# Performance work log

Measured on AMD Instinct MI355X. Metric: run time of the kernel, lower is better.

Reference implementation:

```python
import jax, jax.numpy as jnp
import numpy as np

EPS = 1e-8


def _conv3x3(x, w, b):
    # x: [B,Ci,H,W], w: [Co,Ci,3,3], 'SAME' padding (stride 1)
    y = jax.lax.conv_general_dilated(x, w, (1, 1), 'SAME',
        dimension_numbers=('NCHW', 'OIHW', 'NCHW'))
    return y + b[None, :, None, None]


def _box3(x):
    # depthwise 3x3 box-sum with zero padding (uniform-kernel masked conv)
    C = x.shape[1]
    k = jnp.ones((C, 1, 3, 3), x.dtype)
    return jax.lax.conv_general_dilated(x, k, (1, 1), 'SAME',
        dimension_numbers=('NCHW', 'OIHW', 'NCHW'), feature_group_count=C)


def _unfold3(x):
    # stack_channel(1,9,k=3,p=1): x [B,1,H,W] -> 9 shifted copies [B,9,H,W]
    H, W = x.shape[-2:]
    xp = jnp.pad(x, ((0, 0), (0, 0), (1, 1), (1, 1)))
    return jnp.concatenate([xp[:, :, i:i + H, j:j + W]
                            for i in range(3) for j in range(3)], axis=1)


def _entropy(x):
    # generate_entropy: sigmoid(neighbor - center) averaged over the 3x3 patch
    # x: [B,1,H,W] -> [B,H,W]
    return jax.nn.sigmoid(_unfold3(x) - x).mean(axis=1)


def _pwf(x, params):
    # PixelWeightedFusionSoftmax: 1x1-conv + ReLU chain 2C->128->32->8->1
    for w, b in params:
        x = jax.nn.relu(jnp.einsum('oc,bchw->bohw', w, x) + b[None, :, None, None])
    return x


def _forward(bevs, compress_w, compress_b, pwf_params):
    BT, N, C, H, W = bevs.shape
    tg = bevs[:, 0]                                    # ego agent  [BT,C,H,W]
    nb = bevs[:, 1:].reshape(BT * (N - 1), C, H, W)    # neighbors

    # myCompressNet: 64 -> 1 channel
    tg_com = jax.nn.relu(_conv3x3(tg, compress_w, compress_b))   # [BT,1,H,W]
    nb_com = jax.nn.relu(_conv3x3(nb, compress_w, compress_b))   # [BT*(N-1),1,H,W]

    tg_ent = _entropy(tg_com)                                    # [BT,H,W]
    nb_ent = _entropy(nb_com).reshape(BT, N - 1, H, W)

    # attention_collaboration: select pixels where neighbor entropy exceeds ego's
    mask = (nb_ent > tg_ent[:, None]).astype(bevs.dtype)         # [BT,N-1,H,W]
    bandwidth = mask.mean()                                      # count / (H*W), averaged

    # conv_mask_uniform / interplot_f: partial conv w/ uniform 3x3 kernel
    m = mask.reshape(BT * (N - 1), 1, H, W)
    num = _box3(nb * m)                                          # [BT*(N-1),C,H,W]
    den = _box3(m)
    inter = num / (den + EPS)
    warp = m * nb + (1.0 - m) * inter

    # all-zero neighbors (min+max==0) are passed through untouched
    is_zero = (nb.min(axis=(1, 2, 3)) + nb.max(axis=(1, 2, 3))) == 0
    warp = jnp.where(is_zero[:, None, None, None], nb, warp)

    feats = jnp.concatenate([tg[:, None], warp.reshape(BT, N - 1, C, H, W)],
                            axis=1)                              # [BT,N,C,H,W]

    # per-agent pixel weights: exp / sum-exp normalize, then weighted fusion
    cat = jnp.concatenate([jnp.broadcast_to(tg[:, None], feats.shape), feats],
                          axis=2)                                # [BT,N,2C,H,W]
    logits = _pwf(cat.reshape(BT * N, 2 * C, H, W), pwf_params)
    logits = logits.reshape(BT, N, 1, H, W)
    wts = jnp.exp(logits)
    wts = wts / wts.sum(axis=1, keepdims=True)
    fused = (wts * feats).sum(axis=1)                            # [BT,C,H,W]
    return fused, bandwidth


def setup_inputs() -> dict:
    key = jax.random.key(0)
    ks = jax.random.split(key, 6)
    BT, N, C, H, W = 3, 5, 64, 200, 200
    s = 0.05
    return {
        'bevs': jax.random.normal(ks[0], (BT, N, C, H, W), jnp.float32),
        'compress_w': jax.random.normal(ks[1], (1, C, 3, 3), jnp.float32) * s,
        'compress_b': jnp.zeros((1,), jnp.float32),
        'pwf_w1': jax.random.normal(ks[2], (128, 2 * C), jnp.float32) * s,
        'pwf_b1': jnp.zeros((128,), jnp.float32),
        'pwf_w2': jax.random.normal(ks[3], (32, 128), jnp.float32) * s,
        'pwf_b2': jnp.zeros((32,), jnp.float32),
        'pwf_w3': jax.random.normal(ks[4], (8, 32), jnp.float32) * s,
        'pwf_b3': jnp.zeros((8,), jnp.float32),
        'pwf_w4': jax.random.normal(ks[5], (1, 8), jnp.float32) * s,
        'pwf_b4': jnp.zeros((1,), jnp.float32),
    }


def reference(bevs, compress_w, compress_b, pwf_w1, pwf_b1, pwf_w2, pwf_b2,
              pwf_w3, pwf_b3, pwf_w4, pwf_b4):
    pwf = [(pwf_w1, pwf_b1), (pwf_w2, pwf_b2), (pwf_w3, pwf_b3), (pwf_w4, pwf_b4)]
    return _forward(bevs, compress_w, compress_b, pwf)
```

## Files before the change

kernel.cpp:

```cpp
#include <hip/hip_runtime.h>
#include <hip/hip_bf16.h>
#include <math.h>

#define PP 40000
#define HDIM 200
#define WDIM 200
#define NEPS 1e-8f
#define GX 157
#define NPART (GX*12)

#define OFF_COM    0
#define OFF_ENT    (15*PP)
#define OFF_MASK   (30*PP)
#define OFF_DEN    (42*PP)
#define OFF_LOGITS (54*PP)
#define OFF_MISC   (69*PP)
#define OFF_XTG_F  (69*PP + 64)
#define OFF_XFT_F  (OFF_XTG_F + 3*PP*32)
#define OFF_WBF_F  (OFF_XFT_F + 12*PP*32)
#define OFF_CNT_F  (OFF_WBF_F + 10240)
#define WS_NEED ((size_t)(OFF_CNT_F + NPART + 64)*4)

typedef __attribute__((ext_vector_type(8))) short bf16x8;
typedef __attribute__((ext_vector_type(4))) float f32x4;

__device__ __forceinline__ short f2bf(float f){
    __hip_bfloat16 h = __float2bfloat16(f);
    return *reinterpret_cast<short*>(&h);
}
__device__ __forceinline__ float bf2f(short s){
    return __uint_as_float(((unsigned)(unsigned short)s) << 16);
}

__device__ __forceinline__ unsigned f2ord(float f){
    unsigned u = __float_as_uint(f);
    return (u & 0x80000000u) ? ~u : (u | 0x80000000u);
}
__device__ __forceinline__ float ord2f(unsigned u){
    unsigned v = (u & 0x80000000u) ? (u & 0x7fffffffu) : ~u;
    return __uint_as_float(v);
}

__device__ __forceinline__ void tap_setup(int p, int* off, bool* val){
    int h = p / WDIM, w = p - h*WDIM;
#pragma unroll
    for (int ky=0;ky<3;ky++)
#pragma unroll
        for (int kx=0;kx<3;kx++){
            int t = ky*3+kx;
            int hh = h+ky-1, ww = w+kx-1;
            val[t] = (hh>=0)&&(hh<HDIM)&&(ww>=0)&&(ww<WDIM);
            int hc = min(max(hh,0),HDIM-1);
            int wc = min(max(ww,0),WDIM-1);
            off[t] = hc*WDIM+wc;
        }
}

__global__ void k_init(unsigned* misc){
    int t = threadIdx.x;
    if (t < 12) misc[t] = 0xFFFFFFFFu;
    else if (t < 25) misc[t] = 0u;
}

__global__ __launch_bounds__(256) void k_wcvt(const float* __restrict__ w1,
        const float* __restrict__ w2, short* __restrict__ wbf)
{
    int i = blockIdx.x*256 + threadIdx.x;
    if (i < 16384){
        int e = i&7, l = (i>>3)&63, ks = (i>>9)&3, nt = i>>11;
        int ln = l&15, kg = l>>4;
        wbf[i] = f2bf(w1[(nt*16+ln)*128 + ks*32 + kg*8 + e]);
    } else if (i < 20480){
        int j = i - 16384;
        int e = j&7, l = (j>>3)&63, ks = (j>>9)&3, nt2 = j>>11;
        int ln = l&15, kg = l>>4;
        wbf[i] = f2bf(w2[(nt2*16+ln)*128 + ks*32 + kg*8 + e]);
    }
}

__global__ __launch_bounds__(256) void k_csum(const float* __restrict__ bevs,
        const float* __restrict__ cw, unsigned* __restrict__ misc,
        float* __restrict__ z)
{
    int img = blockIdx.y;
    int n = img % 5;
    int idx = blockIdx.x*256 + threadIdx.x;
    bool act = idx < PP/4;
    int p = idx*4;
    float vmin = INFINITY, vmax = -INFINITY;
    f32x4 acc[9];
#pragma unroll
    for (int t=0;t<9;t++) acc[t] = (f32x4){0.f,0.f,0.f,0.f};
    if (act){
        const float* src = bevs + (size_t)img*64*PP;
#pragma unroll 2
        for (int c=0;c<64;c++){
            f32x4 v = *(const f32x4*)&src[(size_t)c*PP + p];
            vmin = fminf(fminf(fminf(vmin, v[0]), fminf(v[1], v[2])), v[3]);
            vmax = fmaxf(fmaxf(fmaxf(vmax, v[0]), fmaxf(v[1], v[2])), v[3]);
#pragma unroll
            for (int t=0;t<9;t++){
                float w = cw[c*9+t];
#pragma unroll
                for (int j=0;j<4;j++) acc[t][j] = fmaf(w, v[j], acc[t][j]);
            }
        }
        float* zimg = z + (size_t)img*9*PP;
#pragma unroll
        for (int t=0;t<9;t++)
            *(f32x4*)&zimg[(size_t)t*PP + p] = acc[t];
    }
    if (n > 0){
#pragma unroll
        for (int s=32;s>0;s>>=1){
            vmin = fminf(vmin, __shfl_xor(vmin, s, 64));
            vmax = fmaxf(vmax, __shfl_xor(vmax, s, 64));
        }
        if ((threadIdx.x & 63) == 0){
            int im12 = (img/5)*4 + (n-1);
            atomicMin(&misc[im12], f2ord(vmin));
            atomicMax(&misc[12+im12], f2ord(vmax));
        }
    }
}

__global__ __launch_bounds__(256) void k_cfin(const float* __restrict__ z,
        const float* __restrict__ cb, float* __restrict__ com)
{
    int img = blockIdx.y;
    int p = blockIdx.x*256 + threadIdx.x;
    if (p >= PP) return;
    int off[9]; bool val[9];
    tap_setup(p, off, val);
    const float* zimg = z + (size_t)img*9*PP;
    float v[9];
#pragma unroll
    for (int t=0;t<9;t++) v[t] = zimg[(size_t)t*PP + off[t]];
    float acc = cb[0];
#pragma unroll
    for (int t=0;t<9;t++) acc += val[t] ? v[t] : 0.0f;
    com[(size_t)img*PP + p] = fmaxf(acc, 0.0f);
}

__global__ __launch_bounds__(256) void k_conv(const float* __restrict__ bevs,
        const float* __restrict__ cw, const float* __restrict__ cb,
        float* __restrict__ com, unsigned* __restrict__ misc)
{
    int img = blockIdx.y;
    int n = img % 5;
    int p = blockIdx.x*256 + threadIdx.x;
    float vmin = INFINITY, vmax = -INFINITY;
    if (p < PP){
        int off[9]; bool val[9];
        tap_setup(p, off, val);
        const float* src = bevs + (size_t)img*64*PP;
        float acc = cb[0];
#pragma unroll 2
        for (int c=0;c<64;c++){
            const float* sc = src + (size_t)c*PP;
            float v[9];
#pragma unroll
            for (int t=0;t<9;t++) v[t] = sc[off[t]];
            vmin = fminf(vmin, v[4]); vmax = fmaxf(vmax, v[4]);
#pragma unroll
            for (int t=0;t<9;t++)
                acc = fmaf(cw[c*9+t], val[t] ? v[t] : 0.0f, acc);
        }
        com[(size_t)img*PP + p] = fmaxf(acc, 0.0f);
    }
    if (n > 0){
#pragma unroll
        for (int s=32;s>0;s>>=1){
            vmin = fminf(vmin, __shfl_xor(vmin, s, 64));
            vmax = fmaxf(vmax, __shfl_xor(vmax, s, 64));
        }
        if ((threadIdx.x & 63) == 0){
            int im12 = (img/5)*4 + (n-1);
            atomicMin(&misc[im12], f2ord(vmin));
            atomicMax(&misc[12+im12], f2ord(vmax));
        }
    }
}

__global__ __launch_bounds__(256) void k_ent(const float* __restrict__ com,
        float* __restrict__ ent)
{
    int img = blockIdx.y;
    int p = blockIdx.x*256 + threadIdx.x;
    if (p >= PP) return;
    int off[9]; bool val[9];
    tap_setup(p, off, val);
    const float* s = com + (size_t)img*PP;
    float x = s[p];
    float v[9];
#pragma unroll
    for (int t=0;t<9;t++) v[t] = s[off[t]];
    float acc = 0.0f;
#pragma unroll
    for (int t=0;t<9;t++){
        float xv = val[t] ? v[t] : 0.0f;
        acc += 1.0f/(1.0f + expf(x - xv));
    }
    ent[(size_t)img*PP + p] = acc / 9.0f;
}

__global__ __launch_bounds__(256) void k_maskp(const float* __restrict__ ent,
        float* __restrict__ maskb, unsigned* __restrict__ partial)
{
    __shared__ unsigned cnt[4];
    int im12 = blockIdx.y; int bt = im12 >> 2; int n = (im12 & 3) + 1;
    int p = blockIdx.x*256 + threadIdx.x;
    int v = 0;
    if (p < PP){
        float en = ent[(size_t)(bt*5+n)*PP + p];
        float et = ent[(size_t)(bt*5)*PP + p];
        v = en > et;
        maskb[(size_t)im12*PP + p] = (float)v;
    }
    unsigned long long bal = __ballot(v);
    if ((threadIdx.x & 63) == 0) cnt[threadIdx.x>>6] = (unsigned)__popcll(bal);
    __syncthreads();
    if (threadIdx.x == 0)
        partial[blockIdx.y*GX + blockIdx.x] = cnt[0]+cnt[1]+cnt[2]+cnt[3];
}

__global__ __launch_bounds__(256) void k_mask(const float* __restrict__ ent,
        float* __restrict__ maskb, unsigned* __restrict__ misc)
{
    int im12 = blockIdx.y; int bt = im12 >> 2; int n = (im12 & 3) + 1;
    int p = blockIdx.x*256 + threadIdx.x;
    int v = 0;
    if (p < PP){
        float en = ent[(size_t)(bt*5+n)*PP + p];
        float et = ent[(size_t)(bt*5)*PP + p];
        v = en > et;
        maskb[(size_t)im12*PP + p] = (float)v;
    }
    unsigned long long bal = __ballot(v);
    if ((threadIdx.x & 63) == 0) atomicAdd(&misc[24], (unsigned)__popcll(bal));
}

__global__ __launch_bounds__(256) void k_den(const float* __restrict__ maskb,
        float* __restrict__ denb)
{
    int im12 = blockIdx.y;
    int p = blockIdx.x*256 + threadIdx.x;
    if (p >= PP) return;
    int off[9]; bool val[9];
    tap_setup(p, off, val);
    const float* mrow = maskb + (size_t)im12*PP;
    float v[9];
#pragma unroll
    for (int t=0;t<9;t++) v[t] = mrow[off[t]];
    float s = 0.0f;
#pragma unroll
    for (int t=0;t<9;t++) s += val[t] ? v[t] : 0.0f;
    denb[(size_t)im12*PP + p] = s;
}

__global__ __launch_bounds__(256) void k_finp(const unsigned* __restrict__ partial,
        unsigned* misc, float* bwout)
{
    __shared__ unsigned sh[4];
    unsigned s = 0;
    for (int i = threadIdx.x; i < NPART; i += 256) s += partial[i];
#pragma unroll
    for (int sft=32;sft>0;sft>>=1) s += (unsigned)__shfl_xor((int)s, sft, 64);
    if ((threadIdx.x & 63) == 0) sh[threadIdx.x>>6] = s;
    __syncthreads();
    int t = threadIdx.x;
    if (t < 12){
        float mn = ord2f(misc[t]);
        float mx = ord2f(misc[12+t]);
        ((int*)misc)[25+t] = (mn + mx == 0.0f) ? 1 : 0;
    }
    if (t == 12) bwout[0] = (float)(sh[0]+sh[1]+sh[2]+sh[3]) / 480000.0f;
}

__global__ void k_fin(unsigned* misc, float* bwout){
    int t = threadIdx.x;
    if (t < 12){
        float mn = ord2f(misc[t]);
        float mx = ord2f(misc[12+t]);
        ((int*)misc)[25+t] = (mn + mx == 0.0f) ? 1 : 0;
    }
    if (t == 12) bwout[0] = (float)misc[24] / 480000.0f;
}

__global__ __launch_bounds__(256) void k_xtg(const float* __restrict__ bevs,
        short* __restrict__ Xtg)
{
    __shared__ short tile[64][72];
    int tid = threadIdx.x;
    int bt = blockIdx.y;
    int px0 = blockIdx.x*64;
    const float* tg = bevs + (size_t)bt*5*64*PP;
    int c = tid>>2, q = tid&3;
#pragma unroll
    for (int j=0;j<4;j++){
        int pxl = q*16 + j*4;
        f32x4 v = *(const f32x4*)&tg[(size_t)c*PP + px0 + pxl];
#pragma unroll
        for (int e=0;e<4;e++) tile[pxl+e][c] = f2bf(v[e]);
    }
    __syncthreads();
    int pxl = tid&63, qq = tid>>6;
    short* base = Xtg + (size_t)bt*PP*64;
    *(bf16x8*)&base[((size_t)(2*qq  )*PP + px0 + pxl)*8] = *(bf16x8*)&tile[pxl][qq*16];
    *(bf16x8*)&base[((size_t)(2*qq+1)*PP + px0 + pxl)*8] = *(bf16x8*)&tile[pxl][qq*16+8];
}

__global__ __launch_bounds__(256) void k_xft(const float* __restrict__ bevs,
        const float* __restrict__ maskb,
        const unsigned* __restrict__ misc, short* __restrict__ Xft)
{
    int im12 = blockIdx.y; int bt = im12 >> 2; int n = (im12 & 3) + 1;
    int chunk = blockIdx.z;
    int chb = chunk*8;
    int idx = blockIdx.x*256 + threadIdx.x;
    if (idx >= PP/4) return;
    int p = idx*4;
    int row = p / WDIM, col0 = p - row*WDIM;
    int s0 = max(col0-4, 0), s2 = min(col0+4, WDIM-4);
    int rowc[3]; bool rowok[3];
#pragma unroll
    for (int r=0;r<3;r++){
        int rr = row + r - 1;
        rowok[r] = (rr>=0) && (rr<HDIM);
        rowc[r] = min(max(rr,0),HDIM-1) * WDIM;
    }
    bool colok[6];
#pragma unroll
    for (int k=0;k<6;k++){
        int cc = col0 + k - 1;
        colok[k] = (cc>=0) && (cc<WDIM);
    }
    const float* mrow = maskb + (size_t)im12*PP;
    float m6[3][6];
#pragma unroll
    for (int r=0;r<3;r++){
        f32x4 a0 = *(const f32x4*)&mrow[rowc[r] + s0];
        f32x4 a1 = *(const f32x4*)&mrow[rowc[r] + col0];
        f32x4 a2 = *(const f32x4*)&mrow[rowc[r] + s2];
        float mv[6] = {a0[3], a1[0], a1[1], a1[2], a1[3], a2[0]};
#pragma unroll
        for (int k=0;k<6;k++)
            m6[r][k] = (rowok[r] && colok[k]) ? mv[k] : 0.0f;
    }
    float rden[4];
#pragma unroll
    for (int j=0;j<4;j++){
        float d = 0.0f;
#pragma unroll
        for (int r=0;r<3;r++){
#pragma unroll
            for (int dk=0;dk<3;dk++) d += m6[r][j+dk];
        }
        rden[j] = 1.0f/(d + NEPS);
    }
    int iz = ((const int*)misc)[25+im12];
    const float* nbb = bevs + (size_t)(bt*5+n)*64*PP;

    short fv0[8], fv1[8], fv2[8], fv3[8];
#pragma unroll
    for (int ci=0;ci<8;ci++){
        int c = chb + ci;
        const float* sc = nbb + (size_t)c*PP;
        f32x4 v0[3], v1[3], v2[3];
#pragma unroll
        for (int r=0;r<3;r++){
            v0[r] = *(const f32x4*)&sc[rowc[r] + s0];
            v1[r] = *(const f32x4*)&sc[rowc[r] + col0];
            v2[r] = *(const f32x4*)&sc[rowc[r] + s2];
        }
        float num[4];
#pragma unroll
        for (int j=0;j<4;j++) num[j] = 0.0f;
#pragma unroll
        for (int r=0;r<3;r++){
            float vv[6] = {v0[r][3], v1[r][0], v1[r][1], v1[r][2], v1[r][3], v2[r][0]};
#pragma unroll
            for (int j=0;j<4;j++){
#pragma unroll
                for (int dk=0;dk<3;dk++)
                    num[j] = fmaf(m6[r][j+dk], vv[j+dk], num[j]);
            }
        }
        short out4[4];
#pragma unroll
        for (int j=0;j<4;j++){
            float center = v1[1][j];
            float mc = m6[1][j+1];
            float xc = iz ? center : fmaf(mc, center, (1.0f-mc)*(num[j]*rden[j]));
            out4[j] = f2bf(xc);
        }
        fv0[ci]=out4[0]; fv1[ci]=out4[1]; fv2[ci]=out4[2]; fv3[ci]=out4[3];
    }
    short* xc0 = Xft + (size_t)im12*PP*64 + ((size_t)chunk*PP + p)*8;
    *(bf16x8*)&xc0[0]  = *(bf16x8*)&fv0[0];
    *(bf16x8*)&xc0[8]  = *(bf16x8*)&fv1[0];
    *(bf16x8*)&xc0[16] = *(bf16x8*)&fv2[0];
    *(bf16x8*)&xc0[24] = *(bf16x8*)&fv3[0];
}

__global__ __launch_bounds__(256) void k_mlp(const short* __restrict__ Xtg,
        const short* __restrict__ Xft, const short* __restrict__ wbf,
        const float* __restrict__ b1, const float* __restrict__ b2,
        const float* __restrict__ w3, const float* __restrict__ b3,
        const float* __restrict__ w4, const float* __restrict__ b4,
        float* __restrict__ logits)
{
    __shared__ __align__(16) short w1t[16384];
    __shared__ __align__(16) short xt2[4*16*136];
    __shared__ __align__(16) float z2[4*16*33];
    __shared__ float b1l[128], b2l[32], b3l[8], w3l[8*33], w4l[8], b4l[1];

    int tid = threadIdx.x;
    int img = blockIdx.y, bt = img/5, n = img%5;

#pragma unroll
    for (int k=0;k<8;k++){
        int i = tid + k*256;
        *(bf16x8*)&w1t[i*8] = *(const bf16x8*)&wbf[i*8];
    }
    if (tid<256) w3l[(tid>>5)*33 + (tid&31)] = w3[tid];
    if (tid<128) b1l[tid]=b1[tid];
    if (tid<32)  b2l[tid]=b2[tid];
    if (tid<8)   b3l[tid]=b3[tid];
    if (tid<8)   w4l[tid]=w4[tid];
    if (tid==0)  b4l[0]=b4[0];

    int w = tid>>6, l = tid&63;
    int ln = l&15, kg = l>>4;

    bf16x8 w2f[2][4];
#pragma unroll
    for (int nt2=0;nt2<2;nt2++)
#pragma unroll
    for (int ks=0;ks<4;ks++)
        w2f[nt2][ks] = *(const bf16x8*)&wbf[16384 + ((nt2*4+ks)*64 + l)*8];

    __syncthreads();

    const short* xtgb = Xtg + (size_t)bt*PP*64;
    const short* xftb = (n>0) ? (Xft + (size_t)(bt*4+n-1)*PP*64) : xtgb;
    short* xt2w = &xt2[w*16*136];
    float* z2w  = &z2[w*16*33];
    int px_base = blockIdx.x*256 + w*64;

#pragma unroll 1
    for (int mt=0; mt<4; mt++){
        int prow = px_base + mt*16;
        int arow = prow + ln; if (arow > PP-1) arow = PP-1;
        bf16x8 af[4];
        af[0] = *(const bf16x8*)&xtgb[((size_t)kg*PP     + arow)*8];
        af[1] = *(const bf16x8*)&xtgb[((size_t)(kg+4)*PP + arow)*8];
        af[2] = *(const bf16x8*)&xftb[((size_t)kg*PP     + arow)*8];
        af[3] = *(const bf16x8*)&xftb[((size_t)(kg+4)*PP + arow)*8];

#pragma unroll
        for (int nt=0;nt<8;nt++){
            float bias = b1l[nt*16 + ln];
            f32x4 acc = {bias, bias, bias, bias};
#pragma unroll
            for (int ks=0;ks<4;ks++){
                bf16x8 bf = *(const bf16x8*)&w1t[((nt*4+ks)*64 + l)*8];
                acc = __builtin_amdgcn_mfma_f32_16x16x32_bf16(af[ks], bf, acc, 0, 0, 0);
            }
#pragma unroll
            for (int r=0;r<4;r++)
                xt2w[(kg*4+r)*136 + nt*16 + ln] = f2bf(fmaxf(acc[r], 0.0f));
        }

        bf16x8 a2[4];
#pragma unroll
        for (int ks=0;ks<4;ks++)
            a2[ks] = *(const bf16x8*)&xt2w[ln*136 + ks*32 + kg*8];
#pragma unroll
        for (int nt2=0;nt2<2;nt2++){
            float bias = b2l[nt2*16 + ln];
            f32x4 acc = {bias, bias, bias, bias};
#pragma unroll
            for (int ks=0;ks<4;ks++)
                acc = __builtin_amdgcn_mfma_f32_16x16x32_bf16(a2[ks], w2f[nt2][ks], acc, 0, 0, 0);
#pragma unroll
            for (int r=0;r<4;r++)
                z2w[(kg*4+r)*33 + nt2*16 + ln] = fmaxf(acc[r], 0.0f);
        }

        int k0 = kg*2, k1 = kg*2+1;
        float y0 = b3l[k0], y1 = b3l[k1];
#pragma unroll
        for (int j=0;j<32;j++){
            float v = z2w[ln*33 + j];
            y0 = fmaf(w3l[k0*33+j], v, y0);
            y1 = fmaf(w3l[k1*33+j], v, y1);
        }
        float part = w4l[k0]*fmaxf(y0,0.0f) + w4l[k1]*fmaxf(y1,0.0f);
        part += __shfl_xor(part, 16, 64);
        part += __shfl_xor(part, 32, 64);
        if (kg == 0 && prow + ln < PP)
            logits[(size_t)img*PP + prow + ln] = fmaxf(part + b4l[0], 0.0f);
    }
}

__global__ __launch_bounds__(256) void k_fuse2(const float* __restrict__ bevs,
        const float* __restrict__ logits, const short* __restrict__ Xft,
        float* __restrict__ out)
{
    int bt = blockIdx.y;
    int cb = blockIdx.z*32;
    int chunk0 = cb>>3;
    int p = blockIdx.x*256 + threadIdx.x;
    if (p >= PP) return;
    float e[5], ssum = 0.0f;
#pragma unroll
    for (int nn=0;nn<5;nn++){ e[nn] = expf(logits[(size_t)(bt*5+nn)*PP + p]); ssum += e[nn]; }
    float rs = 1.0f/ssum;
    const float* tgb = bevs + (size_t)bt*5*64*PP;
    float acc[32];
    float w0 = e[0]*rs;
#pragma unroll
    for (int ci=0;ci<32;ci++) acc[ci] = w0*tgb[(size_t)(cb+ci)*PP + p];
#pragma unroll
    for (int k=0;k<4;k++){
        float wk = e[k+1]*rs;
        const short* Xim = Xft + (size_t)(bt*4+k)*PP*64;
#pragma unroll
        for (int c8=0;c8<4;c8++){
            bf16x8 v = *(const bf16x8*)&Xim[((size_t)(chunk0+c8)*PP + p)*8];
#pragma unroll
            for (int j=0;j<8;j++)
                acc[c8*8+j] = fmaf(wk, bf2f(v[j]), acc[c8*8+j]);
        }
    }
#pragma unroll
    for (int ci=0;ci<32;ci++)
        out[((size_t)bt*64 + cb+ci)*PP + p] = acc[ci];
}

__global__ __launch_bounds__(256) void k_pwf(const float* __restrict__ bevs,
        const float* __restrict__ w1, const float* __restrict__ b1,
        const float* __restrict__ w2, const float* __restrict__ b2,
        const float* __restrict__ w3, const float* __restrict__ b3,
        const float* __restrict__ w4, const float* __restrict__ b4,
        const float* __restrict__ maskb, const float* __restrict__ denb,
        const unsigned* __restrict__ misc, float* __restrict__ logits)
{
    __shared__ __align__(16) short w1t[128*136];
    __shared__ __align__(16) short w2t[32*136];
    __shared__ __align__(16) short xt[64*136];
    __shared__ __align__(16) float z2[64*33];
    __shared__ float b1l[128], b2l[32], b3l[8], w3l[256], w4l[8], b4l[1];

    int tid = threadIdx.x;
    int img = blockIdx.y, bt = img/5, n = img%5;

    for (int i=tid;i<16384;i+=256) w1t[(i>>7)*136 + (i&127)] = f2bf(w1[i]);
    for (int i=tid;i<4096;i+=256)  w2t[(i>>7)*136 + (i&127)] = f2bf(w2[i]);
    if (tid<128) b1l[tid]=b1[tid];
    if (tid<32)  b2l[tid]=b2[tid];
    if (tid<8)   b3l[tid]=b3[tid];
    if (tid<256) w3l[tid]=w3[tid];
    if (tid<8)   w4l[tid]=w4[tid];
    if (tid==0)  b4l[0]=b4[0];

    int px = tid&63, q = tid>>6;
    int p = blockIdx.x*64 + px;
    const float* tg = bevs + (size_t)bt*5*64*PP;
    if (n == 0){
#pragma unroll
        for (int ci=0;ci<16;ci++){
            int c = q*16+ci;
            short v = f2bf(tg[(size_t)c*PP + p]);
            xt[px*136 + c] = v;
            xt[px*136 + 64 + c] = v;
        }
    } else {
        int im12 = bt*4 + (n-1);
        int off[9]; bool val[9];
        tap_setup(p, off, val);
        const float* mrow = maskb + (size_t)im12*PP;
        float m9[9];
#pragma unroll
        for (int t=0;t<9;t++) m9[t] = val[t] ? mrow[off[t]] : 0.0f;
        float rden = 1.0f/(denb[(size_t)im12*PP + p] + NEPS);
        int iz = ((const int*)misc)[25+im12];
        float mc = m9[4];
        const float* nbb = bevs + (size_t)(bt*5+n)*64*PP;
#pragma unroll
        for (int ci=0;ci<16;ci++){
            int c = q*16+ci;
            xt[px*136 + c] = f2bf(tg[(size_t)c*PP + p]);
            const float* sc = nbb + (size_t)c*PP;
            float num = 0.0f, center = 0.0f;
#pragma unroll
            for (int t=0;t<9;t++){
                if (val[t]){
                    float v = sc[off[t]];
                    num = fmaf(m9[t], v, num);
                    if (t==4) center = v;
                }
            }
            float xc = iz ? center : fmaf(mc, center, (1.0f-mc)*(num*rden));
            xt[px*136 + 64 + c] = f2bf(xc);
        }
    }
    __syncthreads();

    int w = tid>>6, l = tid&63;
    int ln = l&15, kg = l>>4;
    bf16x8 af[4];
#pragma unroll
    for (int ks=0;ks<4;ks++)
        af[ks] = *(const bf16x8*)&xt[(w*16+ln)*136 + ks*32 + kg*8];
#pragma unroll
    for (int nt=0;nt<8;nt++){
        float bias = b1l[nt*16 + ln];
        f32x4 acc = {bias, bias, bias, bias};
#pragma unroll
        for (int ks=0;ks<4;ks++){
            bf16x8 bf = *(const bf16x8*)&w1t[(nt*16+ln)*136 + ks*32 + kg*8];
            acc = __builtin_amdgcn_mfma_f32_16x16x32_bf16(af[ks], bf, acc, 0, 0, 0);
        }
#pragma unroll
        for (int r=0;r<4;r++){
            int pr = w*16 + kg*4 + r;
            xt[pr*136 + nt*16 + ln] = f2bf(fmaxf(acc[r], 0.0f));
        }
    }
    bf16x8 a2[4];
#pragma unroll
    for (int ks=0;ks<4;ks++)
        a2[ks] = *(const bf16x8*)&xt[(w*16+ln)*136 + ks*32 + kg*8];
#pragma unroll
    for (int nt2=0;nt2<2;nt2++){
        float bias = b2l[nt2*16 + ln];
        f32x4 acc = {bias, bias, bias, bias};
#pragma unroll
        for (int ks=0;ks<4;ks++){
            bf16x8 bf = *(const bf16x8*)&w2t[(nt2*16+ln)*136 + ks*32 + kg*8];
            acc = __builtin_amdgcn_mfma_f32_16x16x32_bf16(a2[ks], bf, acc, 0, 0, 0);
        }
#pragma unroll
        for (int r=0;r<4;r++){
            int pr = w*16 + kg*4 + r;
            z2[pr*33 + nt2*16 + ln] = fmaxf(acc[r], 0.0f);
        }
    }
    __syncthreads();
    if (tid < 64){
        float y3[8];
#pragma unroll
        for (int k=0;k<8;k++) y3[k] = b3l[k];
        for (int j=0;j<32;j++){
            float v = z2[tid*33 + j];
#pragma unroll
            for (int k=0;k<8;k++) y3[k] = fmaf(w3l[k*32+j], v, y3[k]);
        }
        float sres = b4l[0];
#pragma unroll
        for (int k=0;k<8;k++) sres = fmaf(w4l[k], fmaxf(y3[k], 0.0f), sres);
        logits[(size_t)img*PP + blockIdx.x*64 + tid] = fmaxf(sres, 0.0f);
    }
}

__global__ __launch_bounds__(256) void k_fuse_old(const float* __restrict__ bevs,
        const float* __restrict__ logits, const float* __restrict__ maskb,
        const float* __restrict__ denb, const unsigned* __restrict__ misc,
        float* __restrict__ out)
{
    int bt = blockIdx.y;
    int p = blockIdx.x*256 + threadIdx.x;
    if (p >= PP) return;
    int off[9]; bool val[9];
    tap_setup(p, off, val);
    float e[5], ssum = 0.0f;
#pragma unroll
    for (int nn=0;nn<5;nn++){ e[nn] = expf(logits[(size_t)(bt*5+nn)*PP + p]); ssum += e[nn]; }
    float wts[5];
#pragma unroll
    for (int nn=0;nn<5;nn++) wts[nn] = e[nn] / ssum;
    float m9[4][9]; float rden[4]; int iz[4];
#pragma unroll
    for (int k=0;k<4;k++){
        int im12 = bt*4 + k;
        const float* mrow = maskb + (size_t)im12*PP;
#pragma unroll
        for (int t=0;t<9;t++) m9[k][t] = val[t] ? mrow[off[t]] : 0.0f;
        rden[k] = 1.0f/(denb[(size_t)im12*PP + p] + NEPS);
        iz[k] = ((const int*)misc)[25+im12];
    }
    const float* base = bevs + (size_t)bt*5*64*PP;
    for (int c=0;c<64;c++){
        float tgc = base[(size_t)c*PP + p];
        float fused = wts[0]*tgc;
#pragma unroll
        for (int k=0;k<4;k++){
            const float* sc = base + (size_t)(k+1)*64*PP + (size_t)c*PP;
            float num = 0.0f, center = 0.0f;
#pragma unroll
            for (int t=0;t<9;t++){
                if (val[t]){
                    float v = sc[off[t]];
                    num = fmaf(m9[k][t], v, num);
                    if (t==4) center = v;
                }
            }
            float mc = m9[k][4];
            float xc = iz[k] ? center : fmaf(mc, center, (1.0f-mc)*(num*rden[k]));
            fused = fmaf(wts[k+1], xc, fused);
        }
        out[((size_t)bt*64 + c)*PP + p] = fused;
    }
}

extern "C" void kernel_launch(void* const* d_in, const int* in_sizes, int n_in,
                              void* d_out, int out_size, void* d_ws, size_t ws_size,
                              hipStream_t stream)
{
    const float* bevs = (const float*)d_in[0];
    const float* cw  = (const float*)d_in[1];
    const float* cb  = (const float*)d_in[2];
    const float* w1  = (const float*)d_in[3];
    const float* b1  = (const float*)d_in[4];
    const float* w2  = (const float*)d_in[5];
    const float* b2  = (const float*)d_in[6];
    const float* w3  = (const float*)d_in[7];
    const float* b3  = (const float*)d_in[8];
    const float* w4  = (const float*)d_in[9];
    const float* b4  = (const float*)d_in[10];
    float* out = (float*)d_out;
    float* ws = (float*)d_ws;

    float* com    = ws + OFF_COM;
    float* ent    = ws + OFF_ENT;
    float* maskb  = ws + OFF_MASK;
    float* denb   = ws + OFF_DEN;
    float* logits = ws + OFF_LOGITS;
    unsigned* misc = (unsigned*)(ws + OFF_MISC);
    short* Xtg    = (short*)(ws + OFF_XTG_F);
    short* Xft    = (short*)(ws + OFF_XFT_F);
    short* wbf    = (short*)(ws + OFF_WBF_F);
    unsigned* cntp = (unsigned*)(ws + OFF_CNT_F);
    float* z      = (float*)(ws + OFF_XFT_F);

    dim3 blk(256,1,1);
    int gx = GX;
    bool big = ws_size >= WS_NEED;

    k_init<<<dim3(1),dim3(64),0,stream>>>(misc);
    if (big){
        k_wcvt<<<dim3(80),blk,0,stream>>>(w1,w2,wbf);
        k_csum<<<dim3((PP/4+255)/256,15),blk,0,stream>>>(bevs,cw,misc,z);
        k_cfin<<<dim3(gx,15),blk,0,stream>>>(z,cb,com);
        k_xtg <<<dim3(PP/64,3),blk,0,stream>>>(bevs,Xtg);
    } else {
        k_conv<<<dim3(gx,15),blk,0,stream>>>(bevs,cw,cb,com,misc);
    }
    k_ent <<<dim3(gx,15),blk,0,stream>>>(com,ent);
    if (big){
        k_maskp<<<dim3(gx,12),blk,0,stream>>>(ent,maskb,cntp);
        k_finp<<<dim3(1),blk,0,stream>>>(cntp, misc, out + (size_t)3*64*PP);
        k_xft  <<<dim3((PP/4+255)/256,12,8),blk,0,stream>>>(bevs,maskb,misc,Xft);
        k_mlp  <<<dim3(gx,15),blk,0,stream>>>(Xtg,Xft,wbf,b1,b2,w3,b3,w4,b4,logits);
        k_fuse2<<<dim3(gx,3,2),blk,0,stream>>>(bevs,logits,Xft,out);
    } else {
        k_mask<<<dim3(gx,12),blk,0,stream>>>(ent,maskb,misc);
        k_den <<<dim3(gx,12),blk,0,stream>>>(maskb,denb);
        k_fin <<<dim3(1),dim3(64),0,stream>>>(misc, out + (size_t)3*64*PP);
        k_pwf  <<<dim3(PP/64,15),blk,0,stream>>>(bevs,w1,b1,w2,b2,w3,b3,w4,b4,maskb,denb,misc,logits);
        k_fuse_old<<<dim3(gx,3),blk,0,stream>>>(bevs,logits,maskb,denb,misc,out);
    }
}
```

Measured before the change: 245.3 us.

## Fuse ego bf16 transpose into compress-sum kernel and stage mask rows in LDS

The separate k_xtg kernel is removed. The ego-agent bf16 channel-packed tensor is now written from inside k_csum, which already streams every channel of the ego image. This avoids a second full read of the ego features and one kernel launch. k_xft also loads the needed mask rows into shared memory once per block instead of doing three overlapping global vector loads per row per thread, at the cost of extra LDS and a barrier.

```diff
diff --git a/kernel.cpp b/kernel.cpp
--- a/kernel.cpp
+++ b/kernel.cpp
@@ -80,10 +80,10 @@
 
 __global__ __launch_bounds__(256) void k_csum(const float* __restrict__ bevs,
         const float* __restrict__ cw, unsigned* __restrict__ misc,
-        float* __restrict__ z)
+        float* __restrict__ z, short* __restrict__ Xtg)
 {
     int img = blockIdx.y;
-    int n = img % 5;
+    int n = img % 5, bt = img / 5;
     int idx = blockIdx.x*256 + threadIdx.x;
     bool act = idx < PP/4;
     int p = idx*4;
@@ -93,16 +93,32 @@
     for (int t=0;t<9;t++) acc[t] = (f32x4){0.f,0.f,0.f,0.f};
     if (act){
         const float* src = bevs + (size_t)img*64*PP;
-#pragma unroll 2
-        for (int c=0;c<64;c++){
-            f32x4 v = *(const f32x4*)&src[(size_t)c*PP + p];
-            vmin = fminf(fminf(fminf(vmin, v[0]), fminf(v[1], v[2])), v[3]);
-            vmax = fmaxf(fmaxf(fmaxf(vmax, v[0]), fmaxf(v[1], v[2])), v[3]);
-#pragma unroll
-            for (int t=0;t<9;t++){
-                float w = cw[c*9+t];
-#pragma unroll
-                for (int j=0;j<4;j++) acc[t][j] = fmaf(w, v[j], acc[t][j]);
+        short* xb0 = Xtg + (size_t)bt*PP*64 + (size_t)p*8;
+#pragma unroll 1
+        for (int cg=0; cg<8; cg++){
+            short tgs[4][8];
+#pragma unroll
+            for (int ci=0; ci<8; ci++){
+                int c = cg*8 + ci;
+                f32x4 v = *(const f32x4*)&src[(size_t)c*PP + p];
+                vmin = fminf(fminf(fminf(vmin, v[0]), fminf(v[1], v[2])), v[3]);
+                vmax = fmaxf(fmaxf(fmaxf(vmax, v[0]), fmaxf(v[1], v[2])), v[3]);
+#pragma unroll
+                for (int t=0;t<9;t++){
+                    float w = cw[c*9+t];
+#pragma unroll
+                    for (int j=0;j<4;j++) acc[t][j] = fmaf(w, v[j], acc[t][j]);
+                }
+                if (n == 0){
+#pragma unroll
+                    for (int j=0;j<4;j++) tgs[j][ci] = f2bf(v[j]);
+                }
+            }
+            if (n == 0){
+                short* xb = xb0 + (size_t)cg*PP*8;
+#pragma unroll
+                for (int j=0;j<4;j++)
+                    *(bf16x8*)&xb[j*8] = *(bf16x8*)&tgs[j][0];
             }
         }
         float* zimg = z + (size_t)img*9*PP;
@@ -287,41 +303,33 @@
     if (t == 12) bwout[0] = (float)misc[24] / 480000.0f;
 }
 
-__global__ __launch_bounds__(256) void k_xtg(const float* __restrict__ bevs,
-        short* __restrict__ Xtg)
-{
-    __shared__ short tile[64][72];
-    int tid = threadIdx.x;
-    int bt = blockIdx.y;
-    int px0 = blockIdx.x*64;
-    const float* tg = bevs + (size_t)bt*5*64*PP;
-    int c = tid>>2, q = tid&3;
-#pragma unroll
-    for (int j=0;j<4;j++){
-        int pxl = q*16 + j*4;
-        f32x4 v = *(const f32x4*)&tg[(size_t)c*PP + px0 + pxl];
-#pragma unroll
-        for (int e=0;e<4;e++) tile[pxl+e][c] = f2bf(v[e]);
-    }
-    __syncthreads();
-    int pxl = tid&63, qq = tid>>6;
-    short* base = Xtg + (size_t)bt*PP*64;
-    *(bf16x8*)&base[((size_t)(2*qq  )*PP + px0 + pxl)*8] = *(bf16x8*)&tile[pxl][qq*16];
-    *(bf16x8*)&base[((size_t)(2*qq+1)*PP + px0 + pxl)*8] = *(bf16x8*)&tile[pxl][qq*16+8];
-}
-
 __global__ __launch_bounds__(256) void k_xft(const float* __restrict__ bevs,
         const float* __restrict__ maskb,
         const unsigned* __restrict__ misc, short* __restrict__ Xft)
 {
+    __shared__ __align__(16) float mlds[9][WDIM];
     int im12 = blockIdx.y; int bt = im12 >> 2; int n = (im12 & 3) + 1;
     int chunk = blockIdx.z;
     int chb = chunk*8;
-    int idx = blockIdx.x*256 + threadIdx.x;
+    int tid = threadIdx.x;
+    int B0 = blockIdx.x*1024;
+    int r0 = B0 / WDIM;
+    int rlast = min((B0 + 1023) / WDIM, HDIM-1);
+    int NR = rlast - r0 + 3;
+    const float* mrow = maskb + (size_t)im12*PP;
+    for (int i = tid; i < NR*WDIM; i += 256){
+        int lr = i / WDIM, col = i - lr*WDIM;
+        int gr = min(max(r0 - 1 + lr, 0), HDIM-1);
+        mlds[lr][col] = mrow[gr*WDIM + col];
+    }
+    __syncthreads();
+
+    int idx = blockIdx.x*256 + tid;
     if (idx >= PP/4) return;
     int p = idx*4;
     int row = p / WDIM, col0 = p - row*WDIM;
     int s0 = max(col0-4, 0), s2 = min(col0+4, WDIM-4);
+    int cl = max(col0-1, 0), cr = min(col0+4, WDIM-1);
     int rowc[3]; bool rowok[3];
 #pragma unroll
     for (int r=0;r<3;r++){
@@ -335,14 +343,13 @@
         int cc = col0 + k - 1;
         colok[k] = (cc>=0) && (cc<WDIM);
     }
-    const float* mrow = maskb + (size_t)im12*PP;
     float m6[3][6];
 #pragma unroll
     for (int r=0;r<3;r++){
-        f32x4 a0 = *(const f32x4*)&mrow[rowc[r] + s0];
-        f32x4 a1 = *(const f32x4*)&mrow[rowc[r] + col0];
-        f32x4 a2 = *(const f32x4*)&mrow[rowc[r] + s2];
-        float mv[6] = {a0[3], a1[0], a1[1], a1[2], a1[3], a2[0]};
+        const float* lrow = &mlds[row - r0 + r][0];
+        f32x4 a1 = *(const f32x4*)&lrow[col0];
+        float mle = lrow[cl], mri = lrow[cr];
+        float mv[6] = {mle, a1[0], a1[1], a1[2], a1[3], mri};
 #pragma unroll
         for (int k=0;k<6;k++)
             m6[r][k] = (rowok[r] && colok[k]) ? mv[k] : 0.0f;
@@ -752,9 +759,8 @@
     k_init<<<dim3(1),dim3(64),0,stream>>>(misc);
     if (big){
         k_wcvt<<<dim3(80),blk,0,stream>>>(w1,w2,wbf);
-        k_csum<<<dim3((PP/4+255)/256,15),blk,0,stream>>>(bevs,cw,misc,z);
+        k_csum<<<dim3((PP/4+255)/256,15),blk,0,stream>>>(bevs,cw,misc,z,Xtg);
         k_cfin<<<dim3(gx,15),blk,0,stream>>>(z,cb,com);
-        k_xtg <<<dim3(PP/64,3),blk,0,stream>>>(bevs,Xtg);
     } else {
         k_conv<<<dim3(gx,15),blk,0,stream>>>(bevs,cw,cb,com,misc);
     }
```

Result: slower. 255.5 us (+4.2%).

## Split compress-conv channel sum across two halves and stage mask rows in LDS

Applied to the files above, without the earlier changes.

The channel-sum kernel is split along the channel dimension into two grid z-halves, each writing its own partial 9-tap buffer, and the finalize kernel adds the two partials. This doubles the block count of the bandwidth-bound first pass to improve occupancy and latency hiding, at the cost of twice the partial-buffer traffic in the finalize step. Separately, the feature-interpolation kernel now loads the mask rows it needs into shared memory once per block and reads its 3x3 neighborhood from there instead of issuing overlapping global vector loads.

```diff
diff --git a/kernel.cpp b/kernel.cpp
--- a/kernel.cpp
+++ b/kernel.cpp
@@ -84,6 +84,8 @@
 {
     int img = blockIdx.y;
     int n = img % 5;
+    int half = blockIdx.z;
+    int cbase = half*32;
     int idx = blockIdx.x*256 + threadIdx.x;
     bool act = idx < PP/4;
     int p = idx*4;
@@ -94,7 +96,8 @@
     if (act){
         const float* src = bevs + (size_t)img*64*PP;
 #pragma unroll 2
-        for (int c=0;c<64;c++){
+        for (int ci=0;ci<32;ci++){
+            int c = cbase + ci;
             f32x4 v = *(const f32x4*)&src[(size_t)c*PP + p];
             vmin = fminf(fminf(fminf(vmin, v[0]), fminf(v[1], v[2])), v[3]);
             vmax = fmaxf(fmaxf(fmaxf(vmax, v[0]), fmaxf(v[1], v[2])), v[3]);
@@ -105,7 +108,7 @@
                 for (int j=0;j<4;j++) acc[t][j] = fmaf(w, v[j], acc[t][j]);
             }
         }
-        float* zimg = z + (size_t)img*9*PP;
+        float* zimg = z + ((size_t)half*15 + img)*9*PP;
 #pragma unroll
         for (int t=0;t<9;t++)
             *(f32x4*)&zimg[(size_t)t*PP + p] = acc[t];
@@ -132,10 +135,12 @@
     if (p >= PP) return;
     int off[9]; bool val[9];
     tap_setup(p, off, val);
-    const float* zimg = z + (size_t)img*9*PP;
+    const float* z0 = z + (size_t)img*9*PP;
+    const float* z1 = z + ((size_t)15 + img)*9*PP;
     float v[9];
 #pragma unroll
-    for (int t=0;t<9;t++) v[t] = zimg[(size_t)t*PP + off[t]];
+    for (int t=0;t<9;t++)
+        v[t] = z0[(size_t)t*PP + off[t]] + z1[(size_t)t*PP + off[t]];
     float acc = cb[0];
 #pragma unroll
     for (int t=0;t<9;t++) acc += val[t] ? v[t] : 0.0f;
@@ -314,14 +319,29 @@
         const float* __restrict__ maskb,
         const unsigned* __restrict__ misc, short* __restrict__ Xft)
 {
+    __shared__ __align__(16) float mlds[9][WDIM];
     int im12 = blockIdx.y; int bt = im12 >> 2; int n = (im12 & 3) + 1;
     int chunk = blockIdx.z;
     int chb = chunk*8;
-    int idx = blockIdx.x*256 + threadIdx.x;
+    int tid = threadIdx.x;
+    int B0 = blockIdx.x*1024;
+    int r0 = B0 / WDIM;
+    int rlast = min((B0 + 1023) / WDIM, HDIM-1);
+    int NR = rlast - r0 + 3;
+    const float* mrow = maskb + (size_t)im12*PP;
+    for (int i = tid; i < NR*WDIM; i += 256){
+        int lr = i / WDIM, col = i - lr*WDIM;
+        int gr = min(max(r0 - 1 + lr, 0), HDIM-1);
+        mlds[lr][col] = mrow[gr*WDIM + col];
+    }
+    __syncthreads();
+
+    int idx = blockIdx.x*256 + tid;
     if (idx >= PP/4) return;
     int p = idx*4;
     int row = p / WDIM, col0 = p - row*WDIM;
     int s0 = max(col0-4, 0), s2 = min(col0+4, WDIM-4);
+    int cl = max(col0-1, 0), cr = min(col0+4, WDIM-1);
     int rowc[3]; bool rowok[3];
 #pragma unroll
     for (int r=0;r<3;r++){
@@ -335,14 +355,13 @@
         int cc = col0 + k - 1;
         colok[k] = (cc>=0) && (cc<WDIM);
     }
-    const float* mrow = maskb + (size_t)im12*PP;
     float m6[3][6];
 #pragma unroll
     for (int r=0;r<3;r++){
-        f32x4 a0 = *(const f32x4*)&mrow[rowc[r] + s0];
-        f32x4 a1 = *(const f32x4*)&mrow[rowc[r] + col0];
-        f32x4 a2 = *(const f32x4*)&mrow[rowc[r] + s2];
-        float mv[6] = {a0[3], a1[0], a1[1], a1[2], a1[3], a2[0]};
+        const float* lrow = &mlds[row - r0 + r][0];
+        f32x4 a1 = *(const f32x4*)&lrow[col0];
+        float mle = lrow[cl], mri = lrow[cr];
+        float mv[6] = {mle, a1[0], a1[1], a1[2], a1[3], mri};
 #pragma unroll
         for (int k=0;k<6;k++)
             m6[r][k] = (rowok[r] && colok[k]) ? mv[k] : 0.0f;
@@ -752,7 +771,7 @@
     k_init<<<dim3(1),dim3(64),0,stream>>>(misc);
     if (big){
         k_wcvt<<<dim3(80),blk,0,stream>>>(w1,w2,wbf);
-        k_csum<<<dim3((PP/4+255)/256,15),blk,0,stream>>>(bevs,cw,misc,z);
+        k_csum<<<dim3((PP/4+255)/256,15,2),blk,0,stream>>>(bevs,cw,misc,z);
         k_cfin<<<dim3(gx,15),blk,0,stream>>>(z,cb,com);
         k_xtg <<<dim3(PP/64,3),blk,0,stream>>>(bevs,Xtg);
     } else {
```

Result: slower. 281.9 us (+15.0%).
